# Optimization experiments

Hardware: AMD Instinct MI355X
Metric: run time of the kernel (lower is better)

## Reference

```python
import jax, jax.numpy as jnp
import numpy as np

N_NODES = 100000
N_EDGES = 1600000
IN_C, HID_C, OUT_C = 128, 128, 64
N_LAYERS, K, ALPHA = 4, 10, 0.1
LN_EPS = 1e-5


def setup_inputs() -> dict:
    key = jax.random.key(0)
    k1, k2, k3, k4, k5 = jax.random.split(key, 5)
    x = jax.random.normal(k1, (N_NODES, IN_C), dtype=jnp.float32)
    edge_index = jax.random.randint(k2, (2, N_EDGES), 0, N_NODES, dtype=jnp.int64)
    edge_weight = jax.random.uniform(k3, (N_EDGES,), dtype=jnp.float32)
    # Learned parameters (torch Linear default init scale ~ 1/sqrt(fan_in))
    W_enc = jax.random.normal(k4, (HID_C, IN_C), dtype=jnp.float32) / np.sqrt(IN_C)
    W_dec = jax.random.normal(k5, (OUT_C, HID_C), dtype=jnp.float32) / np.sqrt(HID_C)
    gamma = jnp.ones((HID_C,), dtype=jnp.float32)
    beta = jnp.zeros((HID_C,), dtype=jnp.float32)
    return {"x": x, "edge_index": edge_index, "edge_weight": edge_weight,
            "W_enc": W_enc, "W_dec": W_dec, "gamma": gamma, "beta": beta}


def _layer_norm(z, gamma, beta):
    mu = jnp.mean(z, axis=-1, keepdims=True)
    var = jnp.mean(jnp.square(z - mu), axis=-1, keepdims=True)
    return gamma * (z - mu) * jax.lax.rsqrt(var + LN_EPS) + beta


def _appnp(h, src, dst, w):
    # K-step personalized-pagerank propagation; normalize=False -> raw edge_weight
    x0 = h
    def step(_, z):
        msg = z[src] * w[:, None]                       # [E, HID_C] gather + scale
        agg = jax.ops.segment_sum(msg, dst, num_segments=N_NODES)  # scatter-add
        return (1.0 - ALPHA) * agg + ALPHA * x0
    return jax.lax.fori_loop(0, K, step, h)


def reference(x, edge_index, edge_weight, W_enc, W_dec, gamma, beta):
    src, dst = edge_index[0], edge_index[1]  # message flows source -> target
    h = x @ W_enc.T
    h = jax.nn.gelu(_layer_norm(h, gamma, beta), approximate=False)
    for _ in range(N_LAYERS):
        h = jax.nn.gelu(_appnp(h, src, dst, edge_weight), approximate=False)
        h = _layer_norm(h, gamma, beta)
    out = h @ W_dec.T
    return jnp.squeeze(out)
```

## Files before the change

### kernel.cpp

```cpp
#include <hip/hip_runtime.h>
#include <math.h>

#define N_NODES 100000
#define N_EDGES 1600000
#define IN_C 128
#define HID_C 128
#define OUT_C 64
#define NLAYERS 4
#define KSTEPS 10
#define ALPHA 0.1f
#define LN_EPS 1e-5f

#define SCAN_N (N_NODES + 1)
#define SCAN_BLOCKS ((SCAN_N + 1023) / 1024)
#define EP_CAP 2400000

__device__ __forceinline__ float gelu_exact(float x) {
    return 0.5f * x * (1.0f + erff(x * 0.70710678118654752f));
}

__device__ __forceinline__ unsigned pack_bf16_rne(float a, float b) {
    unsigned ua = __float_as_uint(a);
    unsigned ub = __float_as_uint(b);
    ua = (ua + 0x7fffu + ((ua >> 16) & 1u)) >> 16;
    ub = (ub + 0x7fffu + ((ub >> 16) & 1u)) >> 16;
    return (ub << 16) | ua;
}
__device__ __forceinline__ float bf_lo(unsigned d) { return __uint_as_float(d << 16); }
__device__ __forceinline__ float bf_hi(unsigned d) { return __uint_as_float(d & 0xffff0000u); }

__global__ void count_k(const int* __restrict__ dst, int* __restrict__ counts) {
    int e = blockIdx.x * blockDim.x + threadIdx.x;
    if (e < N_EDGES) atomicAdd(&counts[dst[e]], 1);
}

__global__ __launch_bounds__(1024) void scan1_k(const int* __restrict__ counts,
                                                int* __restrict__ bsum) {
    __shared__ int s[1024];
    int i = blockIdx.x * 1024 + threadIdx.x;
    int c = 0;
    if (i < N_NODES) c = (counts[i] + 7) & ~7;
    s[threadIdx.x] = c;
    __syncthreads();
    for (int off = 512; off; off >>= 1) {
        if (threadIdx.x < off) s[threadIdx.x] += s[threadIdx.x + off];
        __syncthreads();
    }
    if (threadIdx.x == 0) bsum[blockIdx.x] = s[0];
}

__global__ void scan2_k(int* __restrict__ bsum) {
    __shared__ int s[128];
    int t = threadIdx.x;
    s[t] = (t < SCAN_BLOCKS) ? bsum[t] : 0;
    __syncthreads();
    for (int off = 1; off < 128; off <<= 1) {
        int v = (t >= off) ? s[t - off] : 0;
        __syncthreads();
        s[t] += v;
        __syncthreads();
    }
    if (t < SCAN_BLOCKS) bsum[t] = (t == 0) ? 0 : s[t - 1];
}

__global__ __launch_bounds__(1024) void scan3_k(const int* __restrict__ counts,
                                                const int* __restrict__ bsum,
                                                int* __restrict__ row_off,
                                                int* __restrict__ fill_pos) {
    __shared__ int s[1024];
    int i = blockIdx.x * 1024 + threadIdx.x;
    int c = 0;
    if (i < N_NODES) c = (counts[i] + 7) & ~7;
    s[threadIdx.x] = c;
    __syncthreads();
    for (int off = 1; off < 1024; off <<= 1) {
        int v = (threadIdx.x >= off) ? s[threadIdx.x - off] : 0;
        __syncthreads();
        s[threadIdx.x] += v;
        __syncthreads();
    }
    if (i <= N_NODES) {
        int excl = s[threadIdx.x] - c + bsum[blockIdx.x];
        row_off[i] = excl;
        fill_pos[i] = excl;
    }
}

__global__ void bucket_k(const int* __restrict__ src, const int* __restrict__ dst,
                         const float* __restrict__ w,
                         int* __restrict__ fill_pos, int2* __restrict__ ep) {
    int e = blockIdx.x * blockDim.x + threadIdx.x;
    if (e >= N_EDGES) return;
    int d = dst[e];
    int pos = atomicAdd(&fill_pos[d], 1);
    float ws = (1.0f - ALPHA) * w[e];
    ep[pos] = make_int2(src[e] << 6, __float_as_int(ws));
}

__global__ __launch_bounds__(1024) void encoder_k(
        const float* __restrict__ x, const float* __restrict__ Wenc,
        const float* __restrict__ gamma, const float* __restrict__ beta,
        unsigned* __restrict__ H) {
    __shared__ float WT[IN_C * 130];
    __shared__ float XS[16][512];
    for (int i = threadIdx.x; i < IN_C * HID_C; i += 1024) {
        int c = i >> 7, k = i & 127;
        WT[k * 130 + c] = Wenc[i];
    }
    __syncthreads();
    int lane = threadIdx.x & 63;
    int wid  = threadIdx.x >> 6;
    const float2* WT2 = (const float2*)WT;
    float2 gb = ((const float2*)gamma)[lane];
    float2 bb = ((const float2*)beta)[lane];
    int wstride = gridDim.x * 16;
    float* xs = XS[wid];
    for (int grp = blockIdx.x * 16 + wid; grp * 4 < N_NODES; grp += wstride) {
        int r0 = grp * 4;
        const float4* xr = (const float4*)(x + (size_t)r0 * IN_C);
        ((float4*)xs)[lane]      = xr[lane];
        ((float4*)xs)[64 + lane] = xr[64 + lane];
        __builtin_amdgcn_wave_barrier();
        float a0x = 0, a0y = 0, a1x = 0, a1y = 0;
        float a2x = 0, a2y = 0, a3x = 0, a3y = 0;
        const float4* xs4 = (const float4*)xs;
#pragma unroll 4
        for (int k4 = 0; k4 < 32; ++k4) {
            float4 xv0 = xs4[k4];
            float4 xv1 = xs4[32 + k4];
            float4 xv2 = xs4[64 + k4];
            float4 xv3 = xs4[96 + k4];
            int k = k4 * 4;
            float2 w0 = WT2[(k + 0) * 65 + lane];
            float2 w1 = WT2[(k + 1) * 65 + lane];
            float2 w2 = WT2[(k + 2) * 65 + lane];
            float2 w3 = WT2[(k + 3) * 65 + lane];
#define ENC_ROW(ax, ay, xv)                                      \
            ax = fmaf(xv.x, w0.x, ax); ay = fmaf(xv.x, w0.y, ay); \
            ax = fmaf(xv.y, w1.x, ax); ay = fmaf(xv.y, w1.y, ay); \
            ax = fmaf(xv.z, w2.x, ax); ay = fmaf(xv.z, w2.y, ay); \
            ax = fmaf(xv.w, w3.x, ax); ay = fmaf(xv.w, w3.y, ay);
            ENC_ROW(a0x, a0y, xv0)
            ENC_ROW(a1x, a1y, xv1)
            ENC_ROW(a2x, a2y, xv2)
            ENC_ROW(a3x, a3y, xv3)
#undef ENC_ROW
        }
        __builtin_amdgcn_wave_barrier();
#define ENC_EPI(ax, ay, row)                                               \
        {                                                                   \
            float sum = ax + ay;                                            \
            for (int off = 32; off; off >>= 1) sum += __shfl_xor(sum, off); \
            float mu = sum * (1.0f / 128.0f);                               \
            float d0 = ax - mu, d1 = ay - mu;                               \
            float vs = d0 * d0 + d1 * d1;                                   \
            for (int off = 32; off; off >>= 1) vs += __shfl_xor(vs, off);   \
            float inv = rsqrtf(vs * (1.0f / 128.0f) + LN_EPS);              \
            float o0 = gelu_exact(gb.x * d0 * inv + bb.x);                  \
            float o1 = gelu_exact(gb.y * d1 * inv + bb.y);                  \
            H[(size_t)(row)*64 + lane] = pack_bf16_rne(o0, o1);             \
        }
        ENC_EPI(a0x, a0y, r0)
        ENC_EPI(a1x, a1y, r0 + 1)
        ENC_EPI(a2x, a2y, r0 + 2)
        ENC_EPI(a3x, a3y, r0 + 3)
#undef ENC_EPI
    }
}

__global__ __launch_bounds__(256) void prop_k(
        const unsigned* __restrict__ zin, const unsigned* __restrict__ x0,
        const int* __restrict__ row_off, const int2* __restrict__ ep,
        unsigned* __restrict__ zout, int fuse_ln,
        const float* __restrict__ gamma, const float* __restrict__ beta) {
    int gw = (blockIdx.x * 256 + threadIdx.x) >> 6;
    if (gw >= N_NODES) return;
    int lane = threadIdx.x & 63;
    int s0 = row_off[gw];
    int s1 = row_off[gw + 1];
    float sx = 0.f, sy = 0.f;
    for (int base = s0; base < s1; base += 64) {
        int cnt = min(64, s1 - base);
        int2 p = make_int2(0, 0);
        if (lane < cnt) p = ep[base + lane];
        for (int j = 0; j < cnt; j += 8) {
            int   o0 = __shfl(p.x, j + 0); float w0 = __int_as_float(__shfl(p.y, j + 0));
            int   o1 = __shfl(p.x, j + 1); float w1 = __int_as_float(__shfl(p.y, j + 1));
            int   o2 = __shfl(p.x, j + 2); float w2 = __int_as_float(__shfl(p.y, j + 2));
            int   o3 = __shfl(p.x, j + 3); float w3 = __int_as_float(__shfl(p.y, j + 3));
            int   o4 = __shfl(p.x, j + 4); float w4 = __int_as_float(__shfl(p.y, j + 4));
            int   o5 = __shfl(p.x, j + 5); float w5 = __int_as_float(__shfl(p.y, j + 5));
            int   o6 = __shfl(p.x, j + 6); float w6 = __int_as_float(__shfl(p.y, j + 6));
            int   o7 = __shfl(p.x, j + 7); float w7 = __int_as_float(__shfl(p.y, j + 7));
            unsigned d0 = zin[o0 + lane];
            unsigned d1 = zin[o1 + lane];
            unsigned d2 = zin[o2 + lane];
            unsigned d3 = zin[o3 + lane];
            unsigned d4 = zin[o4 + lane];
            unsigned d5 = zin[o5 + lane];
            unsigned d6 = zin[o6 + lane];
            unsigned d7 = zin[o7 + lane];
            sx = fmaf(w0, bf_lo(d0), sx); sy = fmaf(w0, bf_hi(d0), sy);
            sx = fmaf(w1, bf_lo(d1), sx); sy = fmaf(w1, bf_hi(d1), sy);
            sx = fmaf(w2, bf_lo(d2), sx); sy = fmaf(w2, bf_hi(d2), sy);
            sx = fmaf(w3, bf_lo(d3), sx); sy = fmaf(w3, bf_hi(d3), sy);
            sx = fmaf(w4, bf_lo(d4), sx); sy = fmaf(w4, bf_hi(d4), sy);
            sx = fmaf(w5, bf_lo(d5), sx); sy = fmaf(w5, bf_hi(d5), sy);
            sx = fmaf(w6, bf_lo(d6), sx); sy = fmaf(w6, bf_hi(d6), sy);
            sx = fmaf(w7, bf_lo(d7), sx); sy = fmaf(w7, bf_hi(d7), sy);
        }
    }
    unsigned xd = x0[(size_t)gw * 64 + lane];
    float zx = fmaf(ALPHA, bf_lo(xd), sx);
    float zy = fmaf(ALPHA, bf_hi(xd), sy);
    unsigned od;
    if (fuse_ln) {
        float h0 = gelu_exact(zx);
        float h1 = gelu_exact(zy);
        float sum = h0 + h1;
        for (int off = 32; off; off >>= 1) sum += __shfl_xor(sum, off);
        float mu = sum * (1.0f / 128.0f);
        float d0 = h0 - mu, d1 = h1 - mu;
        float vs = d0 * d0 + d1 * d1;
        for (int off = 32; off; off >>= 1) vs += __shfl_xor(vs, off);
        float inv = rsqrtf(vs * (1.0f / 128.0f) + LN_EPS);
        float2 gb = ((const float2*)gamma)[lane];
        float2 bb = ((const float2*)beta)[lane];
        od = pack_bf16_rne(gb.x * d0 * inv + bb.x, gb.y * d1 * inv + bb.y);
    } else {
        od = pack_bf16_rne(zx, zy);
    }
    zout[(size_t)gw * 64 + lane] = od;
}

__global__ __launch_bounds__(1024) void decoder_k(
        const unsigned* __restrict__ H, const float* __restrict__ Wdec,
        float* __restrict__ out) {
    __shared__ float WT[HID_C * 65];
    __shared__ unsigned XS[16][256];
    for (int i = threadIdx.x; i < OUT_C * HID_C; i += 1024) {
        int o = i >> 7, k = i & 127;
        WT[k * 65 + o] = Wdec[i];
    }
    __syncthreads();
    int lane = threadIdx.x & 63;
    int wid  = threadIdx.x >> 6;
    int wstride = gridDim.x * 16;
    unsigned* xs = XS[wid];
    for (int grp = blockIdx.x * 16 + wid; grp * 4 < N_NODES; grp += wstride) {
        int r0 = grp * 4;
        const unsigned* hp = H + (size_t)r0 * 64;
        xs[lane]       = hp[lane];
        xs[64 + lane]  = hp[64 + lane];
        xs[128 + lane] = hp[128 + lane];
        xs[192 + lane] = hp[192 + lane];
        __builtin_amdgcn_wave_barrier();
        float a0 = 0, a1 = 0, a2 = 0, a3 = 0;
#pragma unroll 4
        for (int k2 = 0; k2 < 64; ++k2) {
            float w0 = WT[(2 * k2) * 65 + lane];
            float w1 = WT[(2 * k2 + 1) * 65 + lane];
            unsigned u0 = xs[k2];
            unsigned u1 = xs[64 + k2];
            unsigned u2 = xs[128 + k2];
            unsigned u3 = xs[192 + k2];
            a0 = fmaf(bf_lo(u0), w0, a0); a0 = fmaf(bf_hi(u0), w1, a0);
            a1 = fmaf(bf_lo(u1), w0, a1); a1 = fmaf(bf_hi(u1), w1, a1);
            a2 = fmaf(bf_lo(u2), w0, a2); a2 = fmaf(bf_hi(u2), w1, a2);
            a3 = fmaf(bf_lo(u3), w0, a3); a3 = fmaf(bf_hi(u3), w1, a3);
        }
        __builtin_amdgcn_wave_barrier();
        out[(size_t)r0 * OUT_C + lane]       = a0;
        out[(size_t)(r0 + 1) * OUT_C + lane] = a1;
        out[(size_t)(r0 + 2) * OUT_C + lane] = a2;
        out[(size_t)(r0 + 3) * OUT_C + lane] = a3;
    }
}

extern "C" void kernel_launch(void* const* d_in, const int* in_sizes, int n_in,
                              void* d_out, int out_size, void* d_ws, size_t ws_size,
                              hipStream_t stream) {
    const float* x     = (const float*)d_in[0];
    const int*   ei    = (const int*)d_in[1];
    const float* ew    = (const float*)d_in[2];
    const float* Wenc  = (const float*)d_in[3];
    const float* Wdec  = (const float*)d_in[4];
    const float* gamma = (const float*)d_in[5];
    const float* beta  = (const float*)d_in[6];
    float* out = (float*)d_out;

    const int* src = ei;
    const int* dst = ei + N_EDGES;

    char* p = (char*)d_ws;
    auto carve = [&](size_t bytes) -> void* {
        void* r = (void*)p;
        p += (bytes + 255) & ~(size_t)255;
        return r;
    };
    int*  counts  = (int*)carve(SCAN_N * sizeof(int));
    int*  fillpos = (int*)carve(SCAN_N * sizeof(int));
    int*  row_off = (int*)carve(SCAN_N * sizeof(int));
    int*  bsum    = (int*)carve(SCAN_BLOCKS * sizeof(int));
    int2* ep      = (int2*)carve((size_t)EP_CAP * sizeof(int2));
    unsigned* H  = (unsigned*)carve((size_t)N_NODES * 64 * sizeof(unsigned));
    unsigned* ZA = (unsigned*)carve((size_t)N_NODES * 64 * sizeof(unsigned));
    unsigned* ZB = (unsigned*)carve((size_t)N_NODES * 64 * sizeof(unsigned));

    hipMemsetAsync(counts, 0, SCAN_N * sizeof(int), stream);
    hipMemsetAsync(ep, 0, (size_t)EP_CAP * sizeof(int2), stream);
    count_k<<<(N_EDGES + 255) / 256, 256, 0, stream>>>(dst, counts);
    scan1_k<<<SCAN_BLOCKS, 1024, 0, stream>>>(counts, bsum);
    scan2_k<<<1, 128, 0, stream>>>(bsum);
    scan3_k<<<SCAN_BLOCKS, 1024, 0, stream>>>(counts, bsum, row_off, fillpos);
    bucket_k<<<(N_EDGES + 255) / 256, 256, 0, stream>>>(src, dst, ew, fillpos, ep);

    encoder_k<<<512, 1024, 0, stream>>>(x, Wenc, gamma, beta, H);

    const int prop_blocks = (N_NODES + 3) / 4;
    unsigned* bufs[2] = {ZA, ZB};
    for (int l = 0; l < NLAYERS; ++l) {
        const unsigned* zin = H;
        for (int k = 0; k < KSTEPS; ++k) {
            int last = (k == KSTEPS - 1);
            unsigned* zout = last ? H : bufs[k & 1];
            prop_k<<<prop_blocks, 256, 0, stream>>>(zin, H, row_off, ep, zout,
                                                    last, gamma, beta);
            zin = zout;
        }
    }

    decoder_k<<<512, 1024, 0, stream>>>(H, Wdec, out);
}
```

Baseline: 2.860 ms.

## Split each warp into four edge groups with 16-byte vector gathers

The propagation kernel now splits each 64-lane warp into four 16-lane subgroups. Each subgroup handles a different edge and each lane loads 16 bytes (8 bf16 features) of the neighbour row, instead of all lanes walking the same edge with 4-byte loads. The edge offsets are stored as byte offsets (src<<8). Partial sums are combined across subgroups with xor shuffles, and LayerNorm reductions now run over 16 lanes. This aims to raise memory-level parallelism and cut shuffle and instruction overhead in the gather. It relies on row segments being padded to a multiple of 4 edges; otherwise tail edges are dropped.

New measurement: 3.864 ms. +35.1%, slower.

```diff
diff --git a/kernel.cpp b/kernel.cpp
--- a/kernel.cpp
+++ b/kernel.cpp
@@ -94,7 +94,7 @@
     int d = dst[e];
     int pos = atomicAdd(&fill_pos[d], 1);
     float ws = (1.0f - ALPHA) * w[e];
-    ep[pos] = make_int2(src[e] << 6, __float_as_int(ws));
+    ep[pos] = make_int2(src[e] << 8, __float_as_int(ws));
 }
 
 __global__ __launch_bounds__(1024) void encoder_k(
@@ -176,61 +176,97 @@
     int gw = (blockIdx.x * 256 + threadIdx.x) >> 6;
     if (gw >= N_NODES) return;
     int lane = threadIdx.x & 63;
+    int sub  = lane >> 4;
+    int m    = lane & 15;
+    int moff = m * 16;
     int s0 = row_off[gw];
     int s1 = row_off[gw + 1];
-    float sx = 0.f, sy = 0.f;
-    for (int base = s0; base < s1; base += 64) {
-        int cnt = min(64, s1 - base);
-        int2 p = make_int2(0, 0);
-        if (lane < cnt) p = ep[base + lane];
-        for (int j = 0; j < cnt; j += 8) {
-            int   o0 = __shfl(p.x, j + 0); float w0 = __int_as_float(__shfl(p.y, j + 0));
-            int   o1 = __shfl(p.x, j + 1); float w1 = __int_as_float(__shfl(p.y, j + 1));
-            int   o2 = __shfl(p.x, j + 2); float w2 = __int_as_float(__shfl(p.y, j + 2));
-            int   o3 = __shfl(p.x, j + 3); float w3 = __int_as_float(__shfl(p.y, j + 3));
-            int   o4 = __shfl(p.x, j + 4); float w4 = __int_as_float(__shfl(p.y, j + 4));
-            int   o5 = __shfl(p.x, j + 5); float w5 = __int_as_float(__shfl(p.y, j + 5));
-            int   o6 = __shfl(p.x, j + 6); float w6 = __int_as_float(__shfl(p.y, j + 6));
-            int   o7 = __shfl(p.x, j + 7); float w7 = __int_as_float(__shfl(p.y, j + 7));
-            unsigned d0 = zin[o0 + lane];
-            unsigned d1 = zin[o1 + lane];
-            unsigned d2 = zin[o2 + lane];
-            unsigned d3 = zin[o3 + lane];
-            unsigned d4 = zin[o4 + lane];
-            unsigned d5 = zin[o5 + lane];
-            unsigned d6 = zin[o6 + lane];
-            unsigned d7 = zin[o7 + lane];
-            sx = fmaf(w0, bf_lo(d0), sx); sy = fmaf(w0, bf_hi(d0), sy);
-            sx = fmaf(w1, bf_lo(d1), sx); sy = fmaf(w1, bf_hi(d1), sy);
-            sx = fmaf(w2, bf_lo(d2), sx); sy = fmaf(w2, bf_hi(d2), sy);
-            sx = fmaf(w3, bf_lo(d3), sx); sy = fmaf(w3, bf_hi(d3), sy);
-            sx = fmaf(w4, bf_lo(d4), sx); sy = fmaf(w4, bf_hi(d4), sy);
-            sx = fmaf(w5, bf_lo(d5), sx); sy = fmaf(w5, bf_hi(d5), sy);
-            sx = fmaf(w6, bf_lo(d6), sx); sy = fmaf(w6, bf_hi(d6), sy);
-            sx = fmaf(w7, bf_lo(d7), sx); sy = fmaf(w7, bf_hi(d7), sy);
-        }
-    }
-    unsigned xd = x0[(size_t)gw * 64 + lane];
-    float zx = fmaf(ALPHA, bf_lo(xd), sx);
-    float zy = fmaf(ALPHA, bf_hi(xd), sy);
-    unsigned od;
+    float acc[8] = {0, 0, 0, 0, 0, 0, 0, 0};
+    const char* zb = (const char*)zin;
+    for (int base = s0; base < s1; base += 32) {
+        int ng = min(32, s1 - base) >> 2;
+        int2 pp[8];
+        uint4 dd[8];
+#pragma unroll
+        for (int j = 0; j < 8; ++j) {
+            int2 q = make_int2(0, 0);
+            if (j < ng) q = ep[base + 4 * j + sub];
+            pp[j] = q;
+        }
+#pragma unroll
+        for (int j = 0; j < 8; ++j) {
+            uint4 d = make_uint4(0, 0, 0, 0);
+            if (j < ng) d = *(const uint4*)(zb + (pp[j].x + moff));
+            dd[j] = d;
+        }
+#pragma unroll
+        for (int j = 0; j < 8; ++j) {
+            float w = __int_as_float(pp[j].y);
+            acc[0] = fmaf(w, bf_lo(dd[j].x), acc[0]);
+            acc[1] = fmaf(w, bf_hi(dd[j].x), acc[1]);
+            acc[2] = fmaf(w, bf_lo(dd[j].y), acc[2]);
+            acc[3] = fmaf(w, bf_hi(dd[j].y), acc[3]);
+            acc[4] = fmaf(w, bf_lo(dd[j].z), acc[4]);
+            acc[5] = fmaf(w, bf_hi(dd[j].z), acc[5]);
+            acc[6] = fmaf(w, bf_lo(dd[j].w), acc[6]);
+            acc[7] = fmaf(w, bf_hi(dd[j].w), acc[7]);
+        }
+    }
+#pragma unroll
+    for (int i = 0; i < 8; ++i) {
+        acc[i] += __shfl_xor(acc[i], 16);
+        acc[i] += __shfl_xor(acc[i], 32);
+    }
+    const uint4* xrow = (const uint4*)((const char*)x0 + (size_t)gw * 256);
+    uint4 xd = xrow[m];
+    float z[8];
+    z[0] = fmaf(ALPHA, bf_lo(xd.x), acc[0]);
+    z[1] = fmaf(ALPHA, bf_hi(xd.x), acc[1]);
+    z[2] = fmaf(ALPHA, bf_lo(xd.y), acc[2]);
+    z[3] = fmaf(ALPHA, bf_hi(xd.y), acc[3]);
+    z[4] = fmaf(ALPHA, bf_lo(xd.z), acc[4]);
+    z[5] = fmaf(ALPHA, bf_hi(xd.z), acc[5]);
+    z[6] = fmaf(ALPHA, bf_lo(xd.w), acc[6]);
+    z[7] = fmaf(ALPHA, bf_hi(xd.w), acc[7]);
+    uint4 od;
     if (fuse_ln) {
-        float h0 = gelu_exact(zx);
-        float h1 = gelu_exact(zy);
-        float sum = h0 + h1;
-        for (int off = 32; off; off >>= 1) sum += __shfl_xor(sum, off);
+        float h[8];
+#pragma unroll
+        for (int i = 0; i < 8; ++i) h[i] = gelu_exact(z[i]);
+        float sum = 0.f;
+#pragma unroll
+        for (int i = 0; i < 8; ++i) sum += h[i];
+        sum += __shfl_xor(sum, 1);
+        sum += __shfl_xor(sum, 2);
+        sum += __shfl_xor(sum, 4);
+        sum += __shfl_xor(sum, 8);
         float mu = sum * (1.0f / 128.0f);
-        float d0 = h0 - mu, d1 = h1 - mu;
-        float vs = d0 * d0 + d1 * d1;
-        for (int off = 32; off; off >>= 1) vs += __shfl_xor(vs, off);
+        float d[8];
+        float vs = 0.f;
+#pragma unroll
+        for (int i = 0; i < 8; ++i) { d[i] = h[i] - mu; vs += d[i] * d[i]; }
+        vs += __shfl_xor(vs, 1);
+        vs += __shfl_xor(vs, 2);
+        vs += __shfl_xor(vs, 4);
+        vs += __shfl_xor(vs, 8);
         float inv = rsqrtf(vs * (1.0f / 128.0f) + LN_EPS);
-        float2 gb = ((const float2*)gamma)[lane];
-        float2 bb = ((const float2*)beta)[lane];
-        od = pack_bf16_rne(gb.x * d0 * inv + bb.x, gb.y * d1 * inv + bb.y);
+        const float4* g4 = (const float4*)gamma;
+        const float4* b4 = (const float4*)beta;
+        float4 ga = g4[2 * m], gc = g4[2 * m + 1];
+        float4 ba = b4[2 * m], bc = b4[2 * m + 1];
+        od.x = pack_bf16_rne(ga.x * d[0] * inv + ba.x, ga.y * d[1] * inv + ba.y);
+        od.y = pack_bf16_rne(ga.z * d[2] * inv + ba.z, ga.w * d[3] * inv + ba.w);
+        od.z = pack_bf16_rne(gc.x * d[4] * inv + bc.x, gc.y * d[5] * inv + bc.y);
+        od.w = pack_bf16_rne(gc.z * d[6] * inv + bc.z, gc.w * d[7] * inv + bc.w);
     } else {
-        od = pack_bf16_rne(zx, zy);
-    }
-    zout[(size_t)gw * 64 + lane] = od;
+        od.x = pack_bf16_rne(z[0], z[1]);
+        od.y = pack_bf16_rne(z[2], z[3]);
+        od.z = pack_bf16_rne(z[4], z[5]);
+        od.w = pack_bf16_rne(z[6], z[7]);
+    }
+    if (sub == 0) {
+        ((uint4*)((char*)zout + (size_t)gw * 256))[m] = od;
+    }
 }
 
 __global__ __launch_bounds__(1024) void decoder_k(
```
